# Kernel optimization log

Measured on AMD Instinct MI355X. Metric: run time of the kernel, lower is better.

Reference implementation:

```python
import jax, jax.numpy as jnp
from jax import lax
import numpy as np

B, PEP, MHC, V, H, C, K, NH, FLAT = 1024, 15, 44, 21, 9, 3200, 9, 800, 21 * 59
EPS = 1e-5


def setup_inputs() -> dict:
    key = jax.random.key(0)
    ks = jax.random.split(key, 24)
    n = lambda k, s: jax.random.normal(k, s, dtype=jnp.float32) * 0.05
    inp = {
        'pep': jax.random.normal(ks[0], (B, PEP, V), dtype=jnp.float32),
        'mhc': jax.random.normal(ks[1], (B, MHC, V), dtype=jnp.float32),
        # conv module (bias=True inside CapHLA_EL)
        'W1': n(ks[2], (2 * C, V)), 'b1': n(ks[3], (2 * C,)),
        'Wd': n(ks[4], (C, 1, K)), 'bd': n(ks[5], (C,)),
        'bn1_g': jnp.ones((C,), jnp.float32), 'bn1_b': jnp.zeros((C,), jnp.float32),
        'bn1_m': jnp.zeros((C,), jnp.float32), 'bn1_v': jnp.ones((C,), jnp.float32),
        'W2': n(ks[6], (V, C)), 'b2': n(ks[7], (V,)),
        # shared LayerNorm(vocab_size)
        'ln_g': jnp.ones((V,), jnp.float32), 'ln_b': jnp.zeros((V,), jnp.float32),
        # MHA (bias=False)
        'Wq': n(ks[8], (V, V * H)), 'Wk': n(ks[9], (V, V * H)),
        'Wv': n(ks[10], (V, V * H)), 'Wo': n(ks[11], (V * H, V)),
        # feature selection head
        'Wf1': n(ks[12], (FLAT, NH)), 'bf1': n(ks[13], (NH,)),
        'bn2_g': jnp.ones((NH,), jnp.float32), 'bn2_b': jnp.zeros((NH,), jnp.float32),
        'bn2_m': jnp.zeros((NH,), jnp.float32), 'bn2_v': jnp.ones((NH,), jnp.float32),
        'Wf2': n(ks[14], (NH, 64)), 'bf2': n(ks[15], (64,)),
        'Wf3': n(ks[16], (64, 2)), 'bf3': n(ks[17], (2,)),
    }
    return inp


def _ln(x, g, b):
    m = x.mean(-1, keepdims=True)
    v = x.var(-1, keepdims=True)
    return (x - m) * lax.rsqrt(v + EPS) * g + b


def _forward(pep, mhc, W1, b1, Wd, bd, bn1_g, bn1_b, bn1_m, bn1_v, W2, b2,
             ln_g, ln_b, Wq, Wk, Wv, Wo,
             Wf1, bf1, bn2_g, bn2_b, bn2_m, bn2_v, Wf2, bf2, Wf3, bf3):
    X = jnp.concatenate([pep, mhc], axis=1)  # [B, 59, V]
    residual = X
    # ---- convolution module (channels-first) ----
    x = X.transpose(0, 2, 1)                               # [B, V, L]
    x = jnp.einsum('bcl,oc->bol', x, W1) + b1[None, :, None]   # [B, 2C, L]
    a, g = jnp.split(x, 2, axis=1)
    x = a * jax.nn.sigmoid(g)                              # GLU -> [B, C, L]
    x = lax.conv_general_dilated(x, Wd, window_strides=(1,), padding=[((K - 1) // 2, (K - 1) // 2)],
                                 dimension_numbers=('NCH', 'OIH', 'NCH'),
                                 feature_group_count=C) + bd[None, :, None]
    x = (x - bn1_m[None, :, None]) * lax.rsqrt(bn1_v + EPS)[None, :, None] * bn1_g[None, :, None] + bn1_b[None, :, None]
    x = jax.nn.silu(x)
    x = jnp.einsum('bcl,oc->bol', x, W2) + b2[None, :, None]  # [B, V, L]
    X = _ln(residual + x.transpose(0, 2, 1), ln_g, ln_b)
    residual = X
    # ---- multi-head self-attention (head_dim == V) ----
    Bn, S, D = X.shape
    def heads(W):
        return (X @ W).reshape(Bn, S, H, D).transpose(0, 2, 1, 3)  # [B, H, S, D]
    q, k, v = heads(Wq), heads(Wk), heads(Wv)
    scores = jnp.einsum('bhqd,bhkd->bhqk', q, k) / jnp.sqrt(jnp.float32(D))
    attn = jax.nn.softmax(scores, axis=-1)
    o = jnp.einsum('bhqk,bhkd->bhqd', attn, v)
    o = o.transpose(0, 2, 1, 3).reshape(Bn, S, H * D) @ Wo
    X = _ln(residual + o, ln_g, ln_b)
    # ---- feature selection head ----
    h = X.reshape(Bn, -1) @ Wf1 + bf1
    h = jax.nn.silu(h)
    h = (h - bn2_m) * lax.rsqrt(bn2_v + EPS) * bn2_g + bn2_b
    h = jax.nn.relu(h @ Wf2 + bf2)
    return h @ Wf3 + bf3                                   # [B, 2]


def reference(pep, mhc, W1, b1, Wd, bd, bn1_g, bn1_b, bn1_m, bn1_v, W2, b2,
              ln_g, ln_b, Wq, Wk, Wv, Wo,
              Wf1, bf1, bn2_g, bn2_b, bn2_m, bn2_v, Wf2, bf2, Wf3, bf3):
    return _forward(pep, mhc, W1, b1, Wd, bd, bn1_g, bn1_b, bn1_m, bn1_v, W2, b2,
                    ln_g, ln_b, Wq, Wk, Wv, Wo,
                    Wf1, bf1, bn2_g, bn2_b, bn2_m, bn2_v, Wf2, bf2, Wf3, bf3)
```

## Files before the change

kernel.cpp:

```cpp
#include <hip/hip_runtime.h>
#include <hip/hip_bf16.h>

namespace {

constexpr int B   = 1024;
constexpr int PEP = 15;
constexpr int MHCN = 44;
constexpr int S   = 59;
constexpr int V   = 21;
constexpr int C   = 3200;
constexpr int KW  = 9;
constexpr int H   = 9;
constexpr int NH  = 800;
constexpr int SV  = S * V;
constexpr int HD  = H * V;
constexpr int XF  = 1248;
constexpr float EPSF = 1e-5f;
constexpr int CHALF = 25;
constexpr float NLOG2E = -1.4426950408889634f;

typedef __attribute__((ext_vector_type(8))) short short8;
typedef __attribute__((ext_vector_type(4))) float f32x4;
typedef __attribute__((ext_vector_type(2))) float f32x2;

__device__ __forceinline__ float sigm(float x) {
  return __builtin_amdgcn_rcpf(1.f + __expf(-x));
}
__device__ __forceinline__ unsigned short f2bf(float f) {
  unsigned r;
  asm("v_cvt_pk_bf16_f32 %0, %1, %2" : "=v"(r) : "v"(f), "v"(f));
  return (unsigned short)r;
}
__device__ __forceinline__ unsigned pkbf(float a, float b) {
  unsigned r;
  asm("v_cvt_pk_bf16_f32 %0, %1, %2" : "=v"(r) : "v"(a), "v"(b));
  return r;
}
__device__ __forceinline__ float bflo(unsigned d) {
  union { unsigned u; float f; } v; v.u = d << 16; return v.f;
}
__device__ __forceinline__ float bfhi(unsigned d) {
  union { unsigned u; float f; } v; v.u = d & 0xffff0000u; return v.f;
}

__global__ void k_packW(const float* __restrict__ W1, const float* __restrict__ b1,
                        const float* __restrict__ Wd,
                        const float* __restrict__ bd, const float* __restrict__ g,
                        const float* __restrict__ bb, const float* __restrict__ m,
                        const float* __restrict__ vv, const float* __restrict__ W2,
                        const float* __restrict__ Wq, const float* __restrict__ Wk,
                        const float* __restrict__ Wv, const float* __restrict__ Wo,
                        const float* __restrict__ Wf1,
                        unsigned short* __restrict__ FB1, unsigned short* __restrict__ FB2,
                        unsigned short* __restrict__ FQKV, unsigned short* __restrict__ FWo,
                        unsigned short* __restrict__ FWf1, float* __restrict__ TAP) {
  int id = blockIdx.x * 256 + threadIdx.x;
  if (id < 400 * 64) {
    int tau = id >> 6, l = id & 63;
    int ci = tau >> 3, tt = tau & 7;
    int lr = l & 15, lg = l >> 4;
    bool isg = (tt >= 4);
    int row = (!isg) ? (ci * 64 + tt * 16 + lr) : (C + ci * 64 + (tt - 4) * 16 + lr);
    float sc = isg ? NLOG2E : 1.f;
    for (int j = 0; j < 8; ++j) {
      int k = lg * 8 + j;
      float val = (k < V) ? W1[row * V + k] * sc : (k == V ? b1[row] * sc : 0.f);
      FB1[(size_t)tau * 512 + l * 8 + j] = f2bf(val);
    }
  } else if (id < 38400) {
    int id2 = id - 25600;
    int sg = id2 >> 6, l = id2 & 63;
    int ci = sg >> 2, rem = sg & 3, kt = rem >> 1, nt = rem & 1;
    int lr = l & 15, lg = l >> 4;
    int vc = nt * 16 + lr;
    for (int j = 0; j < 8; ++j) {
      int ch = ci * 64 + kt * 32 + lg * 8 + j;
      float val = (vc < V) ? W2[(size_t)vc * C + ch] : 0.f;
      FB2[(size_t)sg * 512 + l * 8 + j] = f2bf(val);
    }
  } else if (id < 41856) {
    int id2 = id - 38400;
    int tile = id2 >> 6, l = id2 & 63;
    int h = tile / 6, rem = tile - h * 6;
    int mat = rem >> 1, nt = rem & 1;
    int lr = l & 15, kg = l >> 4;
    int dcol = nt * 16 + lr;
    const float* W = (mat == 0) ? Wq : (mat == 1) ? Wk : Wv;
    const float scale = (mat == 0) ? 0.21821789023599236f : 1.f;
    for (int j = 0; j < 8; ++j) {
      int u = kg * 8 + j;
      float val = (u < V && dcol < V) ? W[u * HD + h * V + dcol] * scale : 0.f;
      FQKV[(size_t)tile * 512 + l * 8 + j] = f2bf(val);
    }
  } else if (id < 43008) {
    int id2 = id - 41856;
    int tile = id2 >> 6, l = id2 & 63;
    int h = tile >> 1, nt = tile & 1;
    int lr = l & 15, kg = l >> 4;
    int vcol = nt * 16 + lr;
    for (int j = 0; j < 8; ++j) {
      int d = kg * 8 + j;
      float val = (d < V && vcol < V) ? Wo[(h * V + d) * V + vcol] : 0.f;
      FWo[(size_t)tile * 512 + l * 8 + j] = f2bf(val);
    }
  } else if (id < 46208) {
    int c = id - 43008;
    if (c < C) {
      float sc = g[c] * rsqrtf(vv[c] + EPSF);
      for (int k = 0; k < KW; ++k) TAP[c * 12 + k] = Wd[c * KW + k] * sc;
      TAP[c * 12 + 9]  = (bd[c] - m[c]) * sc + bb[c];
      TAP[c * 12 + 10] = 0.f;
      TAP[c * 12 + 11] = 0.f;
    }
  } else if (id < 46208 + 1950 * 64) {
    int id2 = id - 46208;
    int tile = id2 >> 6, l = id2 & 63;
    int ntg = tile / 39, kk = tile - ntg * 39;
    int lr = l & 15, kg = l >> 4;
    int n = ntg * 16 + lr;
    for (int j = 0; j < 8; ++j) {
      int f = kk * 32 + kg * 8 + j;
      float val = (f < SV) ? Wf1[(size_t)f * NH + n] : 0.f;
      FWf1[(size_t)tile * 512 + l * 8 + j] = f2bf(val);
    }
  }
}

constexpr int GST = 74;
__global__ __launch_bounds__(256) void k_conv(
    const float* __restrict__ pep, const float* __restrict__ mhc,
    const unsigned short* __restrict__ FB1, const unsigned short* __restrict__ FB2,
    const float* __restrict__ TAP, float* __restrict__ Yp) {
  __shared__ __align__(16) unsigned char smem[64 * GST * 2 + 4 * 16 * 72 * 2];
  unsigned short* Xbf = reinterpret_cast<unsigned short*>(smem);
  unsigned short* gl  = reinterpret_cast<unsigned short*>(smem);
  unsigned short* Sb  = gl + 64 * GST;
  const int t = threadIdx.x;
  const int b = blockIdx.x >> 1;
  const int half = blockIdx.x & 1;
  const int lane = t & 63;
  const int w = t >> 6;
  const int lr = lane & 15;
  const int lg = lane >> 4;

  {
    const int row = t >> 2, q = t & 3;
    const float* xr = (row < PEP) ? pep + ((size_t)b * PEP + row) * V
                    : (row < S)   ? mhc + ((size_t)b * MHCN + (row - PEP)) * V
                                  : nullptr;
#pragma unroll
    for (int i2 = 0; i2 < 5; ++i2) {
      int c0 = q * 10 + 2 * i2;
      float f0 = (xr && c0 < V) ? xr[c0] : 0.f;
      float f1 = (xr && c0 + 1 < V) ? xr[c0 + 1] : ((xr && c0 + 1 == V) ? 1.f : 0.f);
      *reinterpret_cast<unsigned*>(&Xbf[row * 40 + c0]) = pkbf(f0, f1);
    }
  }
  __syncthreads();

  short8 ax = *reinterpret_cast<const short8*>(&Xbf[(w * 16 + lr) * 40 + lg * 8]);
  __syncthreads();

  for (int i = t; i < 64 * 2; i += 256)
    *reinterpret_cast<unsigned*>(&gl[(i >> 1) * GST + (i & 1) * 2]) = 0u;

  f32x4 acc2[2];
  acc2[0] = (f32x4){0.f, 0.f, 0.f, 0.f};
  acc2[1] = (f32x4){0.f, 0.f, 0.f, 0.f};
  const int mypos = w * 16 + lg * 4;

  unsigned* glw0 = reinterpret_cast<unsigned*>(&gl[lr * GST + 4 + mypos]);
  const unsigned* glr = reinterpret_cast<const unsigned*>(&gl[lane * GST + w * 16]);
  unsigned short* sbw = Sb + w * (16 * 72) + lane;
  const unsigned short* sbr = Sb + w * (16 * 72) + lr * 72 + lg * 8;
  const unsigned short* fb1p = FB1 + (size_t)half * CHALF * 8 * 512 + lane * 8;
  const unsigned short* fb2p = FB2 + (size_t)half * CHALF * 4 * 512 + lane * 8;
  const float* tapp = TAP + ((size_t)half * CHALF * 64 + lane) * 12;
  __syncthreads();

  for (int ci = 0; ci < CHALF; ++ci) {
    f32x4 ga[4], gg[4];
#pragma unroll
    for (int tt = 0; tt < 4; ++tt) {
      short8 bf = *reinterpret_cast<const short8*>(fb1p + tt * 512);
      ga[tt] = __builtin_amdgcn_mfma_f32_16x16x32_bf16(ax, bf, (f32x4){0.f, 0.f, 0.f, 0.f}, 0, 0, 0);
    }
#pragma unroll
    for (int tt = 0; tt < 4; ++tt) {
      short8 bf = *reinterpret_cast<const short8*>(fb1p + (4 + tt) * 512);
      gg[tt] = __builtin_amdgcn_mfma_f32_16x16x32_bf16(ax, bf, (f32x4){0.f, 0.f, 0.f, 0.f}, 0, 0, 0);
    }
    if (w < 3) {
#pragma unroll
      for (int tt = 0; tt < 4; ++tt) {
        unsigned* gw = glw0 + tt * (16 * GST / 2);
        float s0 = __builtin_amdgcn_rcpf(1.f + __builtin_amdgcn_exp2f(gg[tt][0]));
        float s1 = __builtin_amdgcn_rcpf(1.f + __builtin_amdgcn_exp2f(gg[tt][1]));
        float s2 = __builtin_amdgcn_rcpf(1.f + __builtin_amdgcn_exp2f(gg[tt][2]));
        float s3 = __builtin_amdgcn_rcpf(1.f + __builtin_amdgcn_exp2f(gg[tt][3]));
        gw[0] = pkbf(ga[tt][0] * s0, ga[tt][1] * s1);
        gw[1] = pkbf(ga[tt][2] * s2, ga[tt][3] * s3);
      }
    } else {
#pragma unroll
      for (int tt = 0; tt < 4; ++tt) {
        unsigned* gw = glw0 + tt * (16 * GST / 2);
        float g0 = (mypos + 0 < S) ? ga[tt][0] * __builtin_amdgcn_rcpf(1.f + __builtin_amdgcn_exp2f(gg[tt][0])) : 0.f;
        float g1 = (mypos + 1 < S) ? ga[tt][1] * __builtin_amdgcn_rcpf(1.f + __builtin_amdgcn_exp2f(gg[tt][1])) : 0.f;
        float g2 = (mypos + 2 < S) ? ga[tt][2] * __builtin_amdgcn_rcpf(1.f + __builtin_amdgcn_exp2f(gg[tt][2])) : 0.f;
        float g3 = (mypos + 3 < S) ? ga[tt][3] * __builtin_amdgcn_rcpf(1.f + __builtin_amdgcn_exp2f(gg[tt][3])) : 0.f;
        gw[0] = pkbf(g0, g1);
        gw[1] = pkbf(g2, g3);
      }
    }
    __syncthreads();
    {
      const float4 t0 = *reinterpret_cast<const float4*>(tapp);
      const float4 t1 = *reinterpret_cast<const float4*>(tapp + 4);
      const float4 t2 = *reinterpret_cast<const float4*>(tapp + 8);
      const float tap[9] = {t0.x, t0.y, t0.z, t0.w, t1.x, t1.y, t1.z, t1.w, t2.x};
      const float sh = t2.y;
      float gv[24];
#pragma unroll
      for (int i2 = 0; i2 < 12; ++i2) {
        const unsigned d = glr[i2];
        gv[2 * i2]     = bflo(d);
        gv[2 * i2 + 1] = bfhi(d);
      }
      f32x2 q[16];
#pragma unroll
      for (int j = 0; j < 16; ++j) q[j] = (f32x2){gv[j], gv[j + 8]};
#pragma unroll
      for (int i2 = 0; i2 < 8; ++i2) {
        f32x2 ac = (f32x2){sh, sh};
#pragma unroll
        for (int k = 0; k < KW; ++k) {
          f32x2 tk = (f32x2){tap[k], tap[k]};
          ac = ac + q[i2 + k] * tk;
        }
        const float a0 = ac.x, a1 = ac.y;
        const float s0 = a0 * __builtin_amdgcn_rcpf(1.f + __builtin_amdgcn_exp2f(a0 * NLOG2E));
        const float s1 = a1 * __builtin_amdgcn_rcpf(1.f + __builtin_amdgcn_exp2f(a1 * NLOG2E));
        sbw[i2 * 72] = f2bf(s0);
        unsigned short hv = f2bf(s1);
        if (w == 3 && i2 >= 3) hv = 0;
        sbw[(i2 + 8) * 72] = hv;
      }
    }
#pragma unroll
    for (int kt = 0; kt < 2; ++kt) {
      short8 a2f = *reinterpret_cast<const short8*>(sbr + kt * 32);
#pragma unroll
      for (int nt = 0; nt < 2; ++nt) {
        short8 b2f = *reinterpret_cast<const short8*>(fb2p + (kt * 2 + nt) * 512);
        acc2[nt] = __builtin_amdgcn_mfma_f32_16x16x32_bf16(a2f, b2f, acc2[nt], 0, 0, 0);
      }
    }
    __syncthreads();
    fb1p += 8 * 512;
    fb2p += 4 * 512;
    tapp += 64 * 12;
  }

  float* yp = Yp + (size_t)blockIdx.x * SV;
#pragma unroll
  for (int nt = 0; nt < 2; ++nt) {
#pragma unroll
    for (int r = 0; r < 4; ++r) {
      const int pos = mypos + r, vc = nt * 16 + lr;
      if (pos < S && vc < V) yp[pos * V + vc] = acc2[nt][r];
    }
  }
}

__global__ __launch_bounds__(64) void k_ln(
    const float* __restrict__ pep, const float* __restrict__ mhc,
    const float* __restrict__ Yp, const float* __restrict__ b2,
    const float* __restrict__ lng, const float* __restrict__ lnb,
    float* __restrict__ X1) {
  const int t = threadIdx.x;
  const int b = blockIdx.x;
  if (t >= S) return;
  const float* xr = (t < PEP) ? pep + ((size_t)b * PEP + t) * V
                              : mhc + ((size_t)b * MHCN + (t - PEP)) * V;
  const float* y0 = Yp + (size_t)(2 * b) * SV + t * V;
  const float* y1 = y0 + SV;
  float z[V];
  float mn = 0.f;
#pragma unroll
  for (int v = 0; v < V; ++v) {
    z[v] = xr[v] + (y0[v] + y1[v]) + b2[v];
    mn += z[v];
  }
  mn *= (1.f / V);
  float var = 0.f;
#pragma unroll
  for (int v = 0; v < V; ++v) {
    float d = z[v] - mn;
    var = fmaf(d, d, var);
  }
  const float inv = rsqrtf(var * (1.f / V) + EPSF);
#pragma unroll
  for (int v = 0; v < V; ++v)
    X1[(size_t)b * SV + t * V + v] = (z[v] - mn) * inv * lng[v] + lnb[v];
}

__global__ __launch_bounds__(256) void k_attn(
    const float* __restrict__ X1, const unsigned short* __restrict__ FQKV,
    const unsigned short* __restrict__ FWo, const float* __restrict__ lng,
    const float* __restrict__ lnb, unsigned short* __restrict__ X2bf) {
  __shared__ float X1f[64 * 21];
  __shared__ __align__(16) unsigned short Qb[64 * 40];
  __shared__ __align__(16) unsigned short Kb[64 * 40];
  __shared__ __align__(16) unsigned short Vt[32 * 72];
  __shared__ __align__(16) unsigned short Pt[64 * 72];
  __shared__ __align__(16) unsigned short Oh[64 * 40];
  const int t = threadIdx.x;
  const int b = blockIdx.x;
  const int lane = t & 63;
  const int w = t >> 6;
  const int lr = lane & 15;
  const int lg = lane >> 4;
  const int mypos = w * 16 + lg * 4;

  for (int i = t; i < 64 * 21; i += 256)
    X1f[i] = (i < SV) ? X1[(size_t)b * SV + i] : 0.f;
  __syncthreads();

  short8 ax;
  {
    const int rowi = w * 16 + lr;
#pragma unroll
    for (int j = 0; j < 8; ++j) {
      int col = lg * 8 + j;
      ax[j] = (short)((col < V) ? f2bf(X1f[rowi * 21 + col]) : (unsigned short)0);
    }
  }
  f32x4 accw[2];
  accw[0] = (f32x4){0.f, 0.f, 0.f, 0.f};
  accw[1] = (f32x4){0.f, 0.f, 0.f, 0.f};

  for (int h = 0; h < H; ++h) {
    const unsigned short* fq = FQKV + (size_t)(h * 6) * 512;
    f32x4 dq[2], dk[2], dv[2];
#pragma unroll
    for (int nt = 0; nt < 2; ++nt) {
      short8 bq = *reinterpret_cast<const short8*>(fq + (0 + nt) * 512 + lane * 8);
      dq[nt] = __builtin_amdgcn_mfma_f32_16x16x32_bf16(ax, bq, (f32x4){0.f, 0.f, 0.f, 0.f}, 0, 0, 0);
      short8 bk = *reinterpret_cast<const short8*>(fq + (2 + nt) * 512 + lane * 8);
      dk[nt] = __builtin_amdgcn_mfma_f32_16x16x32_bf16(ax, bk, (f32x4){0.f, 0.f, 0.f, 0.f}, 0, 0, 0);
      short8 bv = *reinterpret_cast<const short8*>(fq + (4 + nt) * 512 + lane * 8);
      dv[nt] = __builtin_amdgcn_mfma_f32_16x16x32_bf16(ax, bv, (f32x4){0.f, 0.f, 0.f, 0.f}, 0, 0, 0);
    }
#pragma unroll
    for (int nt = 0; nt < 2; ++nt) {
      const int d = nt * 16 + lr;
#pragma unroll
      for (int r = 0; r < 4; ++r) {
        const int pos = mypos + r;
        Qb[pos * 40 + d] = f2bf(dq[nt][r]);
        Kb[pos * 40 + d] = f2bf(dk[nt][r]);
      }
      *reinterpret_cast<unsigned*>(&Vt[d * 72 + mypos])     = pkbf(dv[nt][0], dv[nt][1]);
      *reinterpret_cast<unsigned*>(&Vt[d * 72 + mypos + 2]) = pkbf(dv[nt][2], dv[nt][3]);
    }
    __syncthreads();

    short8 bqf = *reinterpret_cast<const short8*>(&Qb[(w * 16 + lr) * 40 + lg * 8]);
    f32x4 st[4];
#pragma unroll
    for (int mt = 0; mt < 4; ++mt) {
      short8 akf = *reinterpret_cast<const short8*>(&Kb[(mt * 16 + lr) * 40 + lg * 8]);
      st[mt] = __builtin_amdgcn_mfma_f32_16x16x32_bf16(akf, bqf, (f32x4){0.f, 0.f, 0.f, 0.f}, 0, 0, 0);
    }
    float mx = -1e30f;
#pragma unroll
    for (int mt = 0; mt < 4; ++mt)
#pragma unroll
      for (int r = 0; r < 4; ++r) {
        const int j = mt * 16 + lg * 4 + r;
        float sv = (j < S) ? st[mt][r] : -1e30f;
        st[mt][r] = sv;
        mx = fmaxf(mx, sv);
      }
    mx = fmaxf(mx, __shfl_xor(mx, 16));
    mx = fmaxf(mx, __shfl_xor(mx, 32));
    float sum = 0.f;
#pragma unroll
    for (int mt = 0; mt < 4; ++mt)
#pragma unroll
      for (int r = 0; r < 4; ++r) {
        float e = __expf(st[mt][r] - mx);
        st[mt][r] = e;
        sum += e;
      }
    sum += __shfl_xor(sum, 16);
    sum += __shfl_xor(sum, 32);
#pragma unroll
    for (int mt = 0; mt < 4; ++mt) {
#pragma unroll
      for (int s2 = 0; s2 < 2; ++s2) {
        *reinterpret_cast<unsigned*>(&Pt[(w * 16 + lr) * 72 + mt * 16 + lg * 4 + 2 * s2]) =
            pkbf(st[mt][2 * s2], st[mt][2 * s2 + 1]);
      }
    }
    short8 bp0 = *reinterpret_cast<const short8*>(&Pt[(w * 16 + lr) * 72 + lg * 8]);
    short8 bp1 = *reinterpret_cast<const short8*>(&Pt[(w * 16 + lr) * 72 + 32 + lg * 8]);
    f32x4 ot[2];
    ot[0] = (f32x4){0.f, 0.f, 0.f, 0.f};
    ot[1] = (f32x4){0.f, 0.f, 0.f, 0.f};
#pragma unroll
    for (int mt = 0; mt < 2; ++mt) {
      short8 av0 = *reinterpret_cast<const short8*>(&Vt[(mt * 16 + lr) * 72 + lg * 8]);
      ot[mt] = __builtin_amdgcn_mfma_f32_16x16x32_bf16(av0, bp0, ot[mt], 0, 0, 0);
      short8 av1 = *reinterpret_cast<const short8*>(&Vt[(mt * 16 + lr) * 72 + 32 + lg * 8]);
      ot[mt] = __builtin_amdgcn_mfma_f32_16x16x32_bf16(av1, bp1, ot[mt], 0, 0, 0);
    }
    const float inv = __builtin_amdgcn_rcpf(sum);
#pragma unroll
    for (int mt = 0; mt < 2; ++mt) {
#pragma unroll
      for (int s2 = 0; s2 < 2; ++s2) {
        *reinterpret_cast<unsigned*>(&Oh[(w * 16 + lr) * 40 + mt * 16 + lg * 4 + 2 * s2]) =
            pkbf(ot[mt][2 * s2] * inv, ot[mt][2 * s2 + 1] * inv);
      }
    }
    short8 ao = *reinterpret_cast<const short8*>(&Oh[(w * 16 + lr) * 40 + lg * 8]);
#pragma unroll
    for (int nt = 0; nt < 2; ++nt) {
      short8 bw = *reinterpret_cast<const short8*>(FWo + (size_t)(h * 2 + nt) * 512 + lane * 8);
      accw[nt] = __builtin_amdgcn_mfma_f32_16x16x32_bf16(ao, bw, accw[nt], 0, 0, 0);
    }
    __syncthreads();
  }

#pragma unroll
  for (int r = 0; r < 4; ++r) {
    const int pos = mypos + r;
    const bool v1ok = (lr < 5);
    const float x0 = (pos < S) ? X1f[pos * 21 + lr] : 0.f;
    const float x1 = (v1ok && pos < S) ? X1f[pos * 21 + 16 + lr] : 0.f;
    float z0 = accw[0][r] + x0;
    float z1 = v1ok ? (accw[1][r] + x1) : 0.f;
    float s = z0 + z1;
    s += __shfl_xor(s, 1); s += __shfl_xor(s, 2);
    s += __shfl_xor(s, 4); s += __shfl_xor(s, 8);
    const float mn = s * (1.f / V);
    const float d0 = z0 - mn;
    const float d1 = v1ok ? (z1 - mn) : 0.f;
    float vq = d0 * d0 + d1 * d1;
    vq += __shfl_xor(vq, 1); vq += __shfl_xor(vq, 2);
    vq += __shfl_xor(vq, 4); vq += __shfl_xor(vq, 8);
    const float inv = rsqrtf(vq * (1.f / V) + EPSF);
    if (pos < S) {
      X2bf[(size_t)b * XF + pos * 21 + lr] = f2bf(d0 * inv * lng[lr] + lnb[lr]);
      if (v1ok)
        X2bf[(size_t)b * XF + pos * 21 + 16 + lr] = f2bf(d1 * inv * lng[16 + lr] + lnb[16 + lr]);
    }
  }
  if (t < XF - SV) X2bf[(size_t)b * XF + SV + t] = 0;
}

__global__ __launch_bounds__(256) void k_f1(
    const unsigned short* __restrict__ X2bf, const unsigned short* __restrict__ FWf1,
    const float* __restrict__ bf1, const float* __restrict__ g2,
    const float* __restrict__ bb2, const float* __restrict__ m2,
    const float* __restrict__ v2, float* __restrict__ Hb) {
  const int t = threadIdx.x;
  const int lane = t & 63;
  const int w = t >> 6;
  const int lr = lane & 15;
  const int lg = lane >> 4;
  const int Mb = blockIdx.x * 64;
  const int NbT = blockIdx.y * 5;

  const unsigned short* ap = X2bf + (size_t)(Mb + w * 16 + lr) * XF + lg * 8;
  const unsigned short* bp = FWf1 + (size_t)NbT * 39 * 512 + lane * 8;
  f32x4 acc[5];
#pragma unroll
  for (int nt = 0; nt < 5; ++nt) acc[nt] = (f32x4){0.f, 0.f, 0.f, 0.f};

  for (int kk = 0; kk < 39; ++kk) {
    short8 af = *reinterpret_cast<const short8*>(ap + kk * 32);
#pragma unroll
    for (int nt = 0; nt < 5; ++nt) {
      short8 bf = *reinterpret_cast<const short8*>(bp + ((size_t)nt * 39 + kk) * 512);
      acc[nt] = __builtin_amdgcn_mfma_f32_16x16x32_bf16(af, bf, acc[nt], 0, 0, 0);
    }
  }
#pragma unroll
  for (int nt = 0; nt < 5; ++nt) {
    const int n = (NbT + nt) * 16 + lr;
    const float sc = g2[n] * rsqrtf(v2[n] + EPSF);
    const float sh = bb2[n] - m2[n] * sc;
    const float bias = bf1[n];
#pragma unroll
    for (int r = 0; r < 4; ++r) {
      const int row = Mb + w * 16 + lg * 4 + r;
      float hh = acc[nt][r] + bias;
      hh = fmaf(hh * sigm(hh), sc, sh);
      Hb[(size_t)row * NH + n] = hh;
    }
  }
}

__global__ __launch_bounds__(64) void k_f23(
    const float* __restrict__ Hb, const float* __restrict__ Wf2, const float* __restrict__ bf2,
    const float* __restrict__ Wf3, const float* __restrict__ bf3, float* __restrict__ out) {
  __shared__ __align__(16) float hs[NH];
  const int t = threadIdx.x;
  const int b = blockIdx.x;
  for (int i = t; i < NH; i += 64) hs[i] = Hb[(size_t)b * NH + i];
  __syncthreads();
  float acc = bf2[t];
  for (int n = 0; n < NH; n += 4) {
    const float4 hv = *reinterpret_cast<const float4*>(&hs[n]);
    acc = fmaf(hv.x, Wf2[n * 64 + t], acc);
    acc = fmaf(hv.y, Wf2[(n + 1) * 64 + t], acc);
    acc = fmaf(hv.z, Wf2[(n + 2) * 64 + t], acc);
    acc = fmaf(hv.w, Wf2[(n + 3) * 64 + t], acc);
  }
  const float mid = fmaxf(acc, 0.f);
  float p0 = mid * Wf3[t * 2 + 0];
  float p1 = mid * Wf3[t * 2 + 1];
#pragma unroll
  for (int off = 32; off > 0; off >>= 1) {
    p0 += __shfl_down(p0, off);
    p1 += __shfl_down(p1, off);
  }
  if (t == 0) {
    out[b * 2 + 0] = p0 + bf3[0];
    out[b * 2 + 1] = p1 + bf3[1];
  }
}

}

extern "C" void kernel_launch(void* const* d_in, const int* in_sizes, int n_in,
                              void* d_out, int out_size, void* d_ws, size_t ws_size,
                              hipStream_t stream) {
  const float* pep   = (const float*)d_in[0];
  const float* mhc   = (const float*)d_in[1];
  const float* W1    = (const float*)d_in[2];
  const float* b1    = (const float*)d_in[3];
  const float* Wd    = (const float*)d_in[4];
  const float* bd    = (const float*)d_in[5];
  const float* bn1_g = (const float*)d_in[6];
  const float* bn1_b = (const float*)d_in[7];
  const float* bn1_m = (const float*)d_in[8];
  const float* bn1_v = (const float*)d_in[9];
  const float* W2    = (const float*)d_in[10];
  const float* b2    = (const float*)d_in[11];
  const float* ln_g  = (const float*)d_in[12];
  const float* ln_b  = (const float*)d_in[13];
  const float* Wq    = (const float*)d_in[14];
  const float* Wk    = (const float*)d_in[15];
  const float* Wv    = (const float*)d_in[16];
  const float* Wo    = (const float*)d_in[17];
  const float* Wf1   = (const float*)d_in[18];
  const float* bf1   = (const float*)d_in[19];
  const float* bn2_g = (const float*)d_in[20];
  const float* bn2_b = (const float*)d_in[21];
  const float* bn2_m = (const float*)d_in[22];
  const float* bn2_v = (const float*)d_in[23];
  const float* Wf2   = (const float*)d_in[24];
  const float* bf2   = (const float*)d_in[25];
  const float* Wf3   = (const float*)d_in[26];
  const float* bf3   = (const float*)d_in[27];
  float* out = (float*)d_out;

  float* ws = (float*)d_ws;
  float* X1 = ws;
  unsigned short* X2bf = (unsigned short*)(X1 + (size_t)B * SV);
  float* Hb = (float*)(X2bf + (size_t)B * XF);
  float* TAP = Hb + (size_t)B * NH;
  unsigned short* FB1  = (unsigned short*)(TAP + (size_t)C * 12);
  unsigned short* FB2  = FB1 + (size_t)400 * 512;
  unsigned short* FQKV = FB2 + (size_t)200 * 512;
  unsigned short* FWo  = FQKV + (size_t)54 * 512;
  unsigned short* FWf1 = FWo + (size_t)18 * 512;
  float* Yp = (float*)(FWf1 + (size_t)1950 * 512);

  k_packW<<<669, 256, 0, stream>>>(W1, b1, Wd, bd, bn1_g, bn1_b, bn1_m, bn1_v, W2,
                                   Wq, Wk, Wv, Wo, Wf1, FB1, FB2, FQKV, FWo, FWf1, TAP);
  k_conv<<<2 * B, 256, 0, stream>>>(pep, mhc, FB1, FB2, TAP, Yp);
  k_ln<<<B, 64, 0, stream>>>(pep, mhc, Yp, b2, ln_g, ln_b, X1);
  k_attn<<<B, 256, 0, stream>>>(X1, FQKV, FWo, ln_g, ln_b, X2bf);
  dim3 g5(16, 10);
  k_f1<<<g5, 256, 0, stream>>>(X2bf, FWf1, bf1, bn2_g, bn2_b, bn2_m, bn2_v, Hb);
  k_f23<<<B, 64, 0, stream>>>(Hb, Wf2, bf2, Wf3, bf3, out);
}
```

Before: 259.6 us.

## Double-buffer GLU staging in conv kernel to halve block barriers

```diff
diff --git a/kernel.cpp b/kernel.cpp
--- a/kernel.cpp
+++ b/kernel.cpp
@@ -127,14 +127,100 @@
 }
 
 constexpr int GST = 74;
+
+__device__ __forceinline__ void glu_chunk(const unsigned short* fb1p, unsigned* glw0,
+                                          short8 ax, int w, int mypos) {
+  f32x4 ga[4], gg[4];
+#pragma unroll
+  for (int tt = 0; tt < 4; ++tt) {
+    short8 bf = *reinterpret_cast<const short8*>(fb1p + tt * 512);
+    ga[tt] = __builtin_amdgcn_mfma_f32_16x16x32_bf16(ax, bf, (f32x4){0.f, 0.f, 0.f, 0.f}, 0, 0, 0);
+  }
+#pragma unroll
+  for (int tt = 0; tt < 4; ++tt) {
+    short8 bf = *reinterpret_cast<const short8*>(fb1p + (4 + tt) * 512);
+    gg[tt] = __builtin_amdgcn_mfma_f32_16x16x32_bf16(ax, bf, (f32x4){0.f, 0.f, 0.f, 0.f}, 0, 0, 0);
+  }
+  if (w < 3) {
+#pragma unroll
+    for (int tt = 0; tt < 4; ++tt) {
+      unsigned* gw = glw0 + tt * (16 * GST / 2);
+      float s0 = __builtin_amdgcn_rcpf(1.f + __builtin_amdgcn_exp2f(gg[tt][0]));
+      float s1 = __builtin_amdgcn_rcpf(1.f + __builtin_amdgcn_exp2f(gg[tt][1]));
+      float s2 = __builtin_amdgcn_rcpf(1.f + __builtin_amdgcn_exp2f(gg[tt][2]));
+      float s3 = __builtin_amdgcn_rcpf(1.f + __builtin_amdgcn_exp2f(gg[tt][3]));
+      gw[0] = pkbf(ga[tt][0] * s0, ga[tt][1] * s1);
+      gw[1] = pkbf(ga[tt][2] * s2, ga[tt][3] * s3);
+    }
+  } else {
+#pragma unroll
+    for (int tt = 0; tt < 4; ++tt) {
+      unsigned* gw = glw0 + tt * (16 * GST / 2);
+      float g0 = (mypos + 0 < S) ? ga[tt][0] * __builtin_amdgcn_rcpf(1.f + __builtin_amdgcn_exp2f(gg[tt][0])) : 0.f;
+      float g1 = (mypos + 1 < S) ? ga[tt][1] * __builtin_amdgcn_rcpf(1.f + __builtin_amdgcn_exp2f(gg[tt][1])) : 0.f;
+      float g2 = (mypos + 2 < S) ? ga[tt][2] * __builtin_amdgcn_rcpf(1.f + __builtin_amdgcn_exp2f(gg[tt][2])) : 0.f;
+      float g3 = (mypos + 3 < S) ? ga[tt][3] * __builtin_amdgcn_rcpf(1.f + __builtin_amdgcn_exp2f(gg[tt][3])) : 0.f;
+      gw[0] = pkbf(g0, g1);
+      gw[1] = pkbf(g2, g3);
+    }
+  }
+}
+
+__device__ __forceinline__ void conv_chunk(const unsigned* glr, const float* tapp,
+                                           const unsigned short* fb2p,
+                                           unsigned short* sbw, const unsigned short* sbr,
+                                           int w, f32x4 (&acc2)[2]) {
+  const float4 t0 = *reinterpret_cast<const float4*>(tapp);
+  const float4 t1 = *reinterpret_cast<const float4*>(tapp + 4);
+  const float4 t2 = *reinterpret_cast<const float4*>(tapp + 8);
+  const float tap[9] = {t0.x, t0.y, t0.z, t0.w, t1.x, t1.y, t1.z, t1.w, t2.x};
+  const float sh = t2.y;
+  float gv[24];
+#pragma unroll
+  for (int i2 = 0; i2 < 12; ++i2) {
+    const unsigned d = glr[i2];
+    gv[2 * i2]     = bflo(d);
+    gv[2 * i2 + 1] = bfhi(d);
+  }
+  f32x2 q[16];
+#pragma unroll
+  for (int j = 0; j < 16; ++j) q[j] = (f32x2){gv[j], gv[j + 8]};
+#pragma unroll
+  for (int i2 = 0; i2 < 8; ++i2) {
+    f32x2 ac = (f32x2){sh, sh};
+#pragma unroll
+    for (int k = 0; k < KW; ++k) {
+      f32x2 tk = (f32x2){tap[k], tap[k]};
+      ac = ac + q[i2 + k] * tk;
+    }
+    const float a0 = ac.x, a1 = ac.y;
+    const float s0 = a0 * __builtin_amdgcn_rcpf(1.f + __builtin_amdgcn_exp2f(a0 * NLOG2E));
+    const float s1 = a1 * __builtin_amdgcn_rcpf(1.f + __builtin_amdgcn_exp2f(a1 * NLOG2E));
+    sbw[i2 * 72] = f2bf(s0);
+    unsigned short hv = f2bf(s1);
+    if (w == 3 && i2 >= 3) hv = 0;
+    sbw[(i2 + 8) * 72] = hv;
+  }
+#pragma unroll
+  for (int kt = 0; kt < 2; ++kt) {
+    short8 a2f = *reinterpret_cast<const short8*>(sbr + kt * 32);
+#pragma unroll
+    for (int nt = 0; nt < 2; ++nt) {
+      short8 b2f = *reinterpret_cast<const short8*>(fb2p + (kt * 2 + nt) * 512);
+      acc2[nt] = __builtin_amdgcn_mfma_f32_16x16x32_bf16(a2f, b2f, acc2[nt], 0, 0, 0);
+    }
+  }
+}
+
 __global__ __launch_bounds__(256) void k_conv(
     const float* __restrict__ pep, const float* __restrict__ mhc,
     const unsigned short* __restrict__ FB1, const unsigned short* __restrict__ FB2,
     const float* __restrict__ TAP, float* __restrict__ Yp) {
-  __shared__ __align__(16) unsigned char smem[64 * GST * 2 + 4 * 16 * 72 * 2];
+  __shared__ __align__(16) unsigned char smem[2 * 64 * GST * 2 + 4 * 16 * 72 * 2];
   unsigned short* Xbf = reinterpret_cast<unsigned short*>(smem);
-  unsigned short* gl  = reinterpret_cast<unsigned short*>(smem);
-  unsigned short* Sb  = gl + 64 * GST;
+  unsigned short* glA = reinterpret_cast<unsigned short*>(smem);
+  unsigned short* glB = glA + 64 * GST;
+  unsigned short* Sb  = glB + 64 * GST;
   const int t = threadIdx.x;
   const int b = blockIdx.x >> 1;
   const int half = blockIdx.x & 1;
@@ -161,106 +247,43 @@
   short8 ax = *reinterpret_cast<const short8*>(&Xbf[(w * 16 + lr) * 40 + lg * 8]);
   __syncthreads();
 
-  for (int i = t; i < 64 * 2; i += 256)
-    *reinterpret_cast<unsigned*>(&gl[(i >> 1) * GST + (i & 1) * 2]) = 0u;
+  {
+    const int i = t;
+    unsigned short* buf = (i < 128) ? glA : glB;
+    const int i2 = i & 127;
+    *reinterpret_cast<unsigned*>(&buf[(i2 >> 1) * GST + (i2 & 1) * 2]) = 0u;
+  }
 
   f32x4 acc2[2];
   acc2[0] = (f32x4){0.f, 0.f, 0.f, 0.f};
   acc2[1] = (f32x4){0.f, 0.f, 0.f, 0.f};
   const int mypos = w * 16 + lg * 4;
 
-  unsigned* glw0 = reinterpret_cast<unsigned*>(&gl[lr * GST + 4 + mypos]);
-  const unsigned* glr = reinterpret_cast<const unsigned*>(&gl[lane * GST + w * 16]);
+  unsigned* glwA = reinterpret_cast<unsigned*>(&glA[lr * GST + 4 + mypos]);
+  unsigned* glwB = reinterpret_cast<unsigned*>(&glB[lr * GST + 4 + mypos]);
+  const unsigned* glrA = reinterpret_cast<const unsigned*>(&glA[lane * GST + w * 16]);
+  const unsigned* glrB = reinterpret_cast<const unsigned*>(&glB[lane * GST + w * 16]);
   unsigned short* sbw = Sb + w * (16 * 72) + lane;
   const unsigned short* sbr = Sb + w * (16 * 72) + lr * 72 + lg * 8;
   const unsigned short* fb1p = FB1 + (size_t)half * CHALF * 8 * 512 + lane * 8;
   const unsigned short* fb2p = FB2 + (size_t)half * CHALF * 4 * 512 + lane * 8;
   const float* tapp = TAP + ((size_t)half * CHALF * 64 + lane) * 12;
+
+  glu_chunk(fb1p, glwA, ax, w, mypos);
   __syncthreads();
 
-  for (int ci = 0; ci < CHALF; ++ci) {
-    f32x4 ga[4], gg[4];
-#pragma unroll
-    for (int tt = 0; tt < 4; ++tt) {
-      short8 bf = *reinterpret_cast<const short8*>(fb1p + tt * 512);
-      ga[tt] = __builtin_amdgcn_mfma_f32_16x16x32_bf16(ax, bf, (f32x4){0.f, 0.f, 0.f, 0.f}, 0, 0, 0);
-    }
-#pragma unroll
-    for (int tt = 0; tt < 4; ++tt) {
-      short8 bf = *reinterpret_cast<const short8*>(fb1p + (4 + tt) * 512);
-      gg[tt] = __builtin_amdgcn_mfma_f32_16x16x32_bf16(ax, bf, (f32x4){0.f, 0.f, 0.f, 0.f}, 0, 0, 0);
-    }
-    if (w < 3) {
-#pragma unroll
-      for (int tt = 0; tt < 4; ++tt) {
-        unsigned* gw = glw0 + tt * (16 * GST / 2);
-        float s0 = __builtin_amdgcn_rcpf(1.f + __builtin_amdgcn_exp2f(gg[tt][0]));
-        float s1 = __builtin_amdgcn_rcpf(1.f + __builtin_amdgcn_exp2f(gg[tt][1]));
-        float s2 = __builtin_amdgcn_rcpf(1.f + __builtin_amdgcn_exp2f(gg[tt][2]));
-        float s3 = __builtin_amdgcn_rcpf(1.f + __builtin_amdgcn_exp2f(gg[tt][3]));
-        gw[0] = pkbf(ga[tt][0] * s0, ga[tt][1] * s1);
-        gw[1] = pkbf(ga[tt][2] * s2, ga[tt][3] * s3);
-      }
-    } else {
-#pragma unroll
-      for (int tt = 0; tt < 4; ++tt) {
-        unsigned* gw = glw0 + tt * (16 * GST / 2);
-        float g0 = (mypos + 0 < S) ? ga[tt][0] * __builtin_amdgcn_rcpf(1.f + __builtin_amdgcn_exp2f(gg[tt][0])) : 0.f;
-        float g1 = (mypos + 1 < S) ? ga[tt][1] * __builtin_amdgcn_rcpf(1.f + __builtin_amdgcn_exp2f(gg[tt][1])) : 0.f;
-        float g2 = (mypos + 2 < S) ? ga[tt][2] * __builtin_amdgcn_rcpf(1.f + __builtin_amdgcn_exp2f(gg[tt][2])) : 0.f;
-        float g3 = (mypos + 3 < S) ? ga[tt][3] * __builtin_amdgcn_rcpf(1.f + __builtin_amdgcn_exp2f(gg[tt][3])) : 0.f;
-        gw[0] = pkbf(g0, g1);
-        gw[1] = pkbf(g2, g3);
-      }
-    }
+  for (int p = 0; p < 12; ++p) {
+    glu_chunk(fb1p + 4096, glwB, ax, w, mypos);
+    conv_chunk(glrA, tapp, fb2p, sbw, sbr, w, acc2);
     __syncthreads();
-    {
-      const float4 t0 = *reinterpret_cast<const float4*>(tapp);
-      const float4 t1 = *reinterpret_cast<const float4*>(tapp + 4);
-      const float4 t2 = *reinterpret_cast<const float4*>(tapp + 8);
-      const float tap[9] = {t0.x, t0.y, t0.z, t0.w, t1.x, t1.y, t1.z, t1.w, t2.x};
-      const float sh = t2.y;
-      float gv[24];
-#pragma unroll
-      for (int i2 = 0; i2 < 12; ++i2) {
-        const unsigned d = glr[i2];
-        gv[2 * i2]     = bflo(d);
-        gv[2 * i2 + 1] = bfhi(d);
-      }
-      f32x2 q[16];
-#pragma unroll
-      for (int j = 0; j < 16; ++j) q[j] = (f32x2){gv[j], gv[j + 8]};
-#pragma unroll
-      for (int i2 = 0; i2 < 8; ++i2) {
-        f32x2 ac = (f32x2){sh, sh};
-#pragma unroll
-        for (int k = 0; k < KW; ++k) {
-          f32x2 tk = (f32x2){tap[k], tap[k]};
-          ac = ac + q[i2 + k] * tk;
-        }
-        const float a0 = ac.x, a1 = ac.y;
-        const float s0 = a0 * __builtin_amdgcn_rcpf(1.f + __builtin_amdgcn_exp2f(a0 * NLOG2E));
-        const float s1 = a1 * __builtin_amdgcn_rcpf(1.f + __builtin_amdgcn_exp2f(a1 * NLOG2E));
-        sbw[i2 * 72] = f2bf(s0);
-        unsigned short hv = f2bf(s1);
-        if (w == 3 && i2 >= 3) hv = 0;
-        sbw[(i2 + 8) * 72] = hv;
-      }
-    }
-#pragma unroll
-    for (int kt = 0; kt < 2; ++kt) {
-      short8 a2f = *reinterpret_cast<const short8*>(sbr + kt * 32);
-#pragma unroll
-      for (int nt = 0; nt < 2; ++nt) {
-        short8 b2f = *reinterpret_cast<const short8*>(fb2p + (kt * 2 + nt) * 512);
-        acc2[nt] = __builtin_amdgcn_mfma_f32_16x16x32_bf16(a2f, b2f, acc2[nt], 0, 0, 0);
-      }
-    }
+    glu_chunk(fb1p + 2 * 4096, glwA, ax, w, mypos);
+    conv_chunk(glrB, tapp + 768, fb2p + 2048, sbw, sbr, w, acc2);
     __syncthreads();
-    fb1p += 8 * 512;
-    fb2p += 4 * 512;
-    tapp += 64 * 12;
-  }
+    fb1p += 2 * 4096;
+    fb2p += 2 * 2048;
+    tapp += 2 * 768;
+  }
+  conv_chunk(glrA, tapp, fb2p, sbw, sbr, w, acc2);
 
   float* yp = Yp + (size_t)blockIdx.x * SV;
 #pragma unroll
```

Result: faster. 253.1 us (-2.5%).
